# Kernel tuning notes

Measured on AMD Instinct MI355X. Metric: run time of the kernel, lower is better.

## Reference

```python
import jax, jax.numpy as jnp
import numpy as np

B, T, C = 4, 2048, 1024
H = 16
HD = C // H  # 64


def setup_inputs() -> dict:
    key = jax.random.key(0)
    k1, k2, k3 = jax.random.split(key, 3)
    x = jax.random.normal(k1, (B, T, C), dtype=jnp.float32)
    # learned params (torch Linear y = x @ W.T stored here as [in, out])
    Wqkv = jax.random.normal(k2, (C, 3 * C), dtype=jnp.float32) * (C ** -0.5)
    Wout = jax.random.normal(k3, (C, C), dtype=jnp.float32) * (C ** -0.5)
    bout = jnp.zeros((C,), dtype=jnp.float32)
    causal_mask = jnp.tril(jnp.ones((1, 1, T, T), dtype=bool))
    return {"x": x, "causal_mask": causal_mask, "Wqkv": Wqkv, "Wout": Wout, "bout": bout}


def reference(x, causal_mask, Wqkv, Wout, bout):
    b, t, c = x.shape
    scale = HD ** -0.5
    qkv = x @ Wqkv  # [B,T,3C]
    q, k, v = jnp.split(qkv, 3, axis=-1)
    # [B,T,C] -> [B,H,T,hd]
    q = q.reshape(b, t, H, HD).transpose(0, 2, 1, 3)
    k = k.reshape(b, t, H, HD).transpose(0, 2, 1, 3)
    v = v.reshape(b, t, H, HD).transpose(0, 2, 1, 3)
    att = jnp.einsum("bhqd,bhkd->bhqk", q, k) * scale  # [B,H,T,T]
    att = jnp.where(causal_mask, att, -jnp.inf)
    att = jax.nn.softmax(att, axis=-1)
    # dropout in eval mode == identity
    out = jnp.einsum("bhqk,bhkd->bhqd", att, v)  # [B,H,T,hd]
    out = out.transpose(0, 2, 1, 3).reshape(b, t, c)
    return out @ Wout + bout


if __name__ == "__main__":
    inp = setup_inputs()
    y = jax.jit(reference)(**inp)
    print(y.shape, y.dtype)
```

## Files before the change

kernel.cpp:

```cpp
#include <hip/hip_runtime.h>
#include <hip/hip_bf16.h>
#include <stdint.h>


typedef __bf16 bf16;
typedef __bf16 bf16x4 __attribute__((ext_vector_type(4)));
typedef __bf16 bf16x8 __attribute__((ext_vector_type(8)));
typedef float floatx4 __attribute__((ext_vector_type(4)));

#define MFMA16(a, b, c) __builtin_amdgcn_mfma_f32_16x16x32_bf16(a, b, c, 0, 0, 0)

#if defined(__has_builtin)
#if __has_builtin(__builtin_amdgcn_global_load_lds)
#define HAS_GLL 1
#endif
#endif

#ifdef HAS_GLL
__device__ __forceinline__ void gll16(const bf16* g, bf16* l) {
  __builtin_amdgcn_global_load_lds(
      (const __attribute__((address_space(1))) unsigned int*)g,
      (__attribute__((address_space(3))) unsigned int*)l, 16, 0, 0);
}
#endif

__global__ __launch_bounds__(256)
void convert_x(const float* __restrict__ in, bf16* __restrict__ out) {
  const size_t i = (size_t)blockIdx.x * 256 + threadIdx.x;
  const float4* p = (const float4*)in + i * 2;
  float4 a = p[0], b = p[1];
  bf16x8 v;
  v[0] = (bf16)a.x; v[1] = (bf16)a.y; v[2] = (bf16)a.z; v[3] = (bf16)a.w;
  v[4] = (bf16)b.x; v[5] = (bf16)b.y; v[6] = (bf16)b.z; v[7] = (bf16)b.w;
  *((bf16x8*)out + i) = v;
}

__global__ __launch_bounds__(256)
void transpose_w(const float* __restrict__ W, bf16* __restrict__ Wt, int K, int N) {
  __shared__ bf16 tile[32][33];
  const int k0 = blockIdx.y * 32, n0 = blockIdx.x * 32;
  const int t = threadIdx.x;
  {
    const int r = t >> 3, c4 = (t & 7) * 4;
    float4 v = *(const float4*)(W + (size_t)(k0 + r) * N + n0 + c4);
    tile[r][c4 + 0] = (bf16)v.x;
    tile[r][c4 + 1] = (bf16)v.y;
    tile[r][c4 + 2] = (bf16)v.z;
    tile[r][c4 + 3] = (bf16)v.w;
  }
  __syncthreads();
  {
    const int nr = t >> 3, kc = (t & 7) * 4;
    bf16x4 o;
#pragma unroll
    for (int j = 0; j < 4; ++j) o[j] = tile[kc + j][nr];
    *(bf16x4*)(Wt + (size_t)(n0 + nr) * K + k0 + kc) = o;
  }
}

__global__ __launch_bounds__(256)
void vtrans(const bf16* __restrict__ qkv, bf16* __restrict__ vtp) {
  __shared__ bf16 tile[64][72];
  const int t = threadIdx.x;
  const int kb = blockIdx.x * 64;
  const int bh = blockIdx.y;
  const int b = bh >> 4, h = bh & 15;
  const bf16* Vp = qkv + (size_t)b * 2048 * 3072 + 2048 + h * 64;
#pragma unroll
  for (int i = 0; i < 2; ++i) {
    const int c = t + 256 * i, kk = c >> 3, dg = c & 7;
    *(bf16x8*)(&tile[kk][dg * 8]) =
        *(const bf16x8*)(Vp + (size_t)(kb + kk) * 3072 + dg * 8);
  }
  __syncthreads();
#pragma unroll
  for (int i = 0; i < 2; ++i) {
    const int c = t + 256 * i, d = c >> 3, g = c & 7;
    bf16x8 v;
#pragma unroll
    for (int j = 0; j < 8; ++j) v[j] = tile[g * 8 + j][d];
    *(bf16x8*)(vtp + ((size_t)bh * 64 + d) * 2048 + kb + g * 8) = v;
  }
}

template <bool OUT_BF16>
__global__ __launch_bounds__(256, 3)
void gemm_bt(const bf16* __restrict__ A, const bf16* __restrict__ Bt,
             const float* __restrict__ bias, void* __restrict__ Cv,
             int M, int N, int K) {
  __shared__ __align__(16) bf16 As[128 * 64];
  __shared__ __align__(16) bf16 Bs[128 * 64];

  const int t = threadIdx.x, lane = t & 63, w = t >> 6;
  const int m_ = lane & 15, quad = lane >> 4;
  const int wm = w >> 1, wn = w & 1;
  const int m0 = blockIdx.y * 128, n0 = blockIdx.x * 128;

  floatx4 acc[4][4];
#pragma unroll
  for (int i = 0; i < 4; ++i)
#pragma unroll
    for (int j = 0; j < 4; ++j) {
      floatx4 z = {0.f, 0.f, 0.f, 0.f};
      acc[i][j] = z;
    }

  for (int k0 = 0; k0 < K; k0 += 64) {
#pragma unroll
    for (int i = 0; i < 4; ++i) {
      const int R0 = i * 32 + w * 8;
      const int R = R0 + (lane >> 3);
      const int sg = (lane & 7) ^ (R & 7);
      const bf16* ga = A + (size_t)(m0 + R) * K + k0 + sg * 8;
      const bf16* gb = Bt + (size_t)(n0 + R) * K + k0 + sg * 8;
#ifdef HAS_GLL
      gll16(ga, As + (size_t)R0 * 64);
      gll16(gb, Bs + (size_t)R0 * 64);
#else
      *(bf16x8*)(As + (size_t)R * 64 + (lane & 7) * 8) = *(const bf16x8*)ga;
      *(bf16x8*)(Bs + (size_t)R * 64 + (lane & 7) * 8) = *(const bf16x8*)gb;
#endif
    }
    __syncthreads();

#pragma unroll
    for (int kc = 0; kc < 2; ++kc) {
      bf16x8 af[4], bfr[4];
#pragma unroll
      for (int mt = 0; mt < 4; ++mt) {
        const int r = wm * 64 + mt * 16 + m_;
        const int slot = ((kc << 2) | quad) ^ (r & 7);
        af[mt] = *(const bf16x8*)(As + (size_t)r * 64 + slot * 8);
      }
#pragma unroll
      for (int nt = 0; nt < 4; ++nt) {
        const int rn = wn * 64 + nt * 16 + m_;
        const int slot = ((kc << 2) | quad) ^ (rn & 7);
        bfr[nt] = *(const bf16x8*)(Bs + (size_t)rn * 64 + slot * 8);
      }
#pragma unroll
      for (int mt = 0; mt < 4; ++mt)
#pragma unroll
        for (int nt = 0; nt < 4; ++nt)
          acc[mt][nt] = MFMA16(af[mt], bfr[nt], acc[mt][nt]);
    }
    __syncthreads();
  }

#pragma unroll
  for (int mt = 0; mt < 4; ++mt)
#pragma unroll
    for (int nt = 0; nt < 4; ++nt) {
      const int col = n0 + wn * 64 + nt * 16 + m_;
      const float bv = bias ? bias[col] : 0.f;
#pragma unroll
      for (int r = 0; r < 4; ++r) {
        const int row = m0 + wm * 64 + mt * 16 + quad * 4 + r;
        const float val = acc[mt][nt][r] + bv;
        if (OUT_BF16)
          ((bf16*)Cv)[(size_t)row * N + col] = (bf16)val;
        else
          ((float*)Cv)[(size_t)row * N + col] = val;
      }
    }
}

__global__ __launch_bounds__(256, 2)
void attn_fwd(const bf16* __restrict__ qkv, const bf16* __restrict__ vtp,
              bf16* __restrict__ attnout) {
  constexpr int KS = 72;
  constexpr float L2E = 1.44269504f;
  __shared__ __align__(16) bf16 Ks[64 * KS];
  __shared__ __align__(16) bf16 VT[64 * KS];
  __shared__ __align__(16) bf16 Pl[128 * KS];

  const int t = threadIdx.x, lane = t & 63, w = t >> 6;
  const int m_ = lane & 15, quad = lane >> 4;
  const int bh = blockIdx.x;
  const int pb = blockIdx.y;
  const int b = bh >> 4, h = bh & 15;
  const int srcbase = (lane & 48) + ((lane & 48) >> 2);

  const bf16* base = qkv + (size_t)b * 2048 * 3072;
  const bf16* Qp = base + h * 64;
  const bf16* Kp = base + 1024 + h * 64;
  const bf16* Vt = vtp + (size_t)bh * 64 * 2048;

  const int sr0 = t >> 3, sg0 = t & 7;
  const int sr1 = (t + 256) >> 3, sg1 = t & 7;

#pragma unroll
  for (int pass = 0; pass < 2; ++pass) {
    const int qb = pass ? (15 - pb) : pb;
    const int q0w = qb * 128 + w * 32;

    bf16x8 qf[2][2];
#pragma unroll
    for (int mt = 0; mt < 2; ++mt)
#pragma unroll
      for (int kc = 0; kc < 2; ++kc)
        qf[mt][kc] = *(const bf16x8*)(Qp + (size_t)(q0w + mt * 16 + m_) * 3072 +
                                      kc * 32 + quad * 8);

    floatx4 o[2][4];
#pragma unroll
    for (int mt = 0; mt < 2; ++mt)
#pragma unroll
      for (int nt = 0; nt < 4; ++nt) {
        floatx4 z = {0.f, 0.f, 0.f, 0.f};
        o[mt][nt] = z;
      }
    float mrow[2] = {-1e30f, -1e30f}, lrow[2] = {0.f, 0.f};

    const int nch = 2 * qb + 2;

    bf16x8 kr0, kr1, vr0, vr1;
    kr0 = *(const bf16x8*)(Kp + (size_t)sr0 * 3072 + sg0 * 8);
    kr1 = *(const bf16x8*)(Kp + (size_t)sr1 * 3072 + sg1 * 8);
    vr0 = *(const bf16x8*)(Vt + (size_t)sr0 * 2048 + sg0 * 8);
    vr1 = *(const bf16x8*)(Vt + (size_t)sr1 * 2048 + sg1 * 8);

    for (int ch = 0; ch < nch; ++ch) {
      const int kb = ch * 64;
      __syncthreads();
      *(bf16x8*)(Ks + (size_t)sr0 * KS + sg0 * 8) = kr0;
      *(bf16x8*)(Ks + (size_t)sr1 * KS + sg1 * 8) = kr1;
      *(bf16x8*)(VT + (size_t)sr0 * KS + sg0 * 8) = vr0;
      *(bf16x8*)(VT + (size_t)sr1 * KS + sg1 * 8) = vr1;
      __syncthreads();
      if (ch + 1 < nch) {
        const int kn = kb + 64;
        kr0 = *(const bf16x8*)(Kp + (size_t)(kn + sr0) * 3072 + sg0 * 8);
        kr1 = *(const bf16x8*)(Kp + (size_t)(kn + sr1) * 3072 + sg1 * 8);
        vr0 = *(const bf16x8*)(Vt + (size_t)sr0 * 2048 + kn + sg0 * 8);
        vr1 = *(const bf16x8*)(Vt + (size_t)sr1 * 2048 + kn + sg1 * 8);
      }

      if (kb <= q0w + 31) {
        bf16x8 kf[4][2];
#pragma unroll
        for (int kt = 0; kt < 4; ++kt)
#pragma unroll
          for (int kc = 0; kc < 2; ++kc)
            kf[kt][kc] = *(const bf16x8*)(Ks + (size_t)(kt * 16 + m_) * KS +
                                          kc * 32 + quad * 8);
        const bool need_mask = (kb + 63 > q0w);
#pragma unroll
        for (int mt = 0; mt < 2; ++mt) {
          floatx4 s[4];
#pragma unroll
          for (int kt = 0; kt < 4; ++kt) {
            floatx4 z = {0.f, 0.f, 0.f, 0.f};
            z = MFMA16(kf[kt][0], qf[mt][0], z);
            z = MFMA16(kf[kt][1], qf[mt][1], z);
            s[kt] = z;
          }
          float a[4][4];
#pragma unroll
          for (int kt = 0; kt < 4; ++kt)
#pragma unroll
            for (int r = 0; r < 4; ++r) a[kt][r] = s[kt][r] * (0.125f * L2E);
          if (need_mask) {
            const int qglob = q0w + mt * 16 + m_;
#pragma unroll
            for (int kt = 0; kt < 4; ++kt)
#pragma unroll
              for (int r = 0; r < 4; ++r)
                if (kb + kt * 16 + quad * 4 + r > qglob) a[kt][r] = -1e30f;
          }
          float mx = -1e30f;
#pragma unroll
          for (int kt = 0; kt < 4; ++kt)
#pragma unroll
            for (int r = 0; r < 4; ++r) mx = fmaxf(mx, a[kt][r]);
          mx = fmaxf(mx, __shfl_xor(mx, 16));
          mx = fmaxf(mx, __shfl_xor(mx, 32));
          const float mnew = fmaxf(mrow[mt], mx);
          const float alpha = exp2f(mrow[mt] - mnew);
          mrow[mt] = mnew;
          float psum = 0.f;
#pragma unroll
          for (int kt = 0; kt < 4; ++kt) {
            bf16x4 pw;
#pragma unroll
            for (int r = 0; r < 4; ++r) {
              const float p = exp2f(a[kt][r] - mnew);
              psum += p;
              pw[r] = (bf16)p;
            }
            *(bf16x4*)(Pl + (size_t)((w * 2 + mt) * 16 + m_) * KS + kt * 16 +
                       quad * 4) = pw;
          }
          psum += __shfl_xor(psum, 16);
          psum += __shfl_xor(psum, 32);
          lrow[mt] = lrow[mt] * alpha + psum;
#pragma unroll
          for (int r = 0; r < 4; ++r) {
            const float ar = __shfl(alpha, srcbase + r);
#pragma unroll
            for (int nt = 0; nt < 4; ++nt) o[mt][nt][r] *= ar;
          }
        }
        bf16x8 vf[4][2];
#pragma unroll
        for (int nt = 0; nt < 4; ++nt)
#pragma unroll
          for (int kc = 0; kc < 2; ++kc)
            vf[nt][kc] = *(const bf16x8*)(VT + (size_t)(nt * 16 + m_) * KS +
                                          kc * 32 + quad * 8);
#pragma unroll
        for (int mt = 0; mt < 2; ++mt) {
          const bf16* prow = Pl + (size_t)((w * 2 + mt) * 16 + m_) * KS;
          const bf16x8 pf0 = *(const bf16x8*)(prow + quad * 8);
          const bf16x8 pf1 = *(const bf16x8*)(prow + 32 + quad * 8);
#pragma unroll
          for (int nt = 0; nt < 4; ++nt) {
            o[mt][nt] = MFMA16(pf0, vf[nt][0], o[mt][nt]);
            o[mt][nt] = MFMA16(pf1, vf[nt][1], o[mt][nt]);
          }
        }
      }
    }
    __syncthreads();

#pragma unroll
    for (int mt = 0; mt < 2; ++mt) {
      const float linv = 1.0f / lrow[mt];
#pragma unroll
      for (int r = 0; r < 4; ++r) {
        const float inv = __shfl(linv, srcbase + r);
        const int row = q0w + mt * 16 + quad * 4 + r;
        const size_t orow = ((size_t)b * 2048 + row) * 1024 + h * 64;
#pragma unroll
        for (int nt = 0; nt < 4; ++nt)
          attnout[orow + nt * 16 + m_] = (bf16)(o[mt][nt][r] * inv);
      }
    }
  }
}

extern "C" void kernel_launch(void* const* d_in, const int* in_sizes, int n_in,
                              void* d_out, int out_size, void* d_ws, size_t ws_size,
                              hipStream_t stream) {
  (void)in_sizes; (void)n_in; (void)out_size; (void)ws_size;
  const float* x    = (const float*)d_in[0];
  const float* Wqkv = (const float*)d_in[2];
  const float* Wout = (const float*)d_in[3];
  const float* bout = (const float*)d_in[4];
  float* out = (float*)d_out;

  bf16* qkv     = (bf16*)d_ws;
  bf16* attnout = (bf16*)((char*)d_ws + (size_t)8192 * 3072 * 2);
  bf16* Wout_t  = (bf16*)d_ws;
  bf16* xbf    = (bf16*)d_out;
  bf16* Wqkv_t = (bf16*)d_out + (size_t)8192 * 1024;
  bf16* vtp    = (bf16*)d_out + (size_t)8192 * 1024;

  convert_x<<<4096, 256, 0, stream>>>(x, xbf);
  transpose_w<<<dim3(96, 32), 256, 0, stream>>>(Wqkv, Wqkv_t, 1024, 3072);

  gemm_bt<true><<<dim3(24, 64), 256, 0, stream>>>(xbf, Wqkv_t, nullptr, qkv,
                                                  8192, 3072, 1024);
  vtrans<<<dim3(32, 64), 256, 0, stream>>>(qkv, vtp);
  attn_fwd<<<dim3(64, 8), 256, 0, stream>>>(qkv, vtp, attnout);

  transpose_w<<<dim3(32, 32), 256, 0, stream>>>(Wout, Wout_t, 1024, 1024);
  gemm_bt<false><<<dim3(8, 64), 256, 0, stream>>>(attnout, Wout_t, bout, out,
                                                  8192, 1024, 1024);
}
```

Measured before the change: 281.9 us.

## Fuse V transpose into QKV GEMM epilogue, prescale Q, skip unneeded rescales

The QKV GEMM epilogue now writes Q (prescaled by softmax scale times log2e) and K into a compact buffer and writes V directly in transposed per-head layout, removing the separate vtrans kernel. The attention kernel drops its per-score scaling multiply and only rescales the output accumulator when some row max grew in the wave. The transposed V stores are strided and less coalesced, and prescaling Q before bf16 rounding slightly changes numerics.

```diff
diff --git a/kernel.cpp b/kernel.cpp
--- a/kernel.cpp
+++ b/kernel.cpp
@@ -58,36 +58,11 @@
   }
 }
 
-__global__ __launch_bounds__(256)
-void vtrans(const bf16* __restrict__ qkv, bf16* __restrict__ vtp) {
-  __shared__ bf16 tile[64][72];
-  const int t = threadIdx.x;
-  const int kb = blockIdx.x * 64;
-  const int bh = blockIdx.y;
-  const int b = bh >> 4, h = bh & 15;
-  const bf16* Vp = qkv + (size_t)b * 2048 * 3072 + 2048 + h * 64;
-#pragma unroll
-  for (int i = 0; i < 2; ++i) {
-    const int c = t + 256 * i, kk = c >> 3, dg = c & 7;
-    *(bf16x8*)(&tile[kk][dg * 8]) =
-        *(const bf16x8*)(Vp + (size_t)(kb + kk) * 3072 + dg * 8);
-  }
-  __syncthreads();
-#pragma unroll
-  for (int i = 0; i < 2; ++i) {
-    const int c = t + 256 * i, d = c >> 3, g = c & 7;
-    bf16x8 v;
-#pragma unroll
-    for (int j = 0; j < 8; ++j) v[j] = tile[g * 8 + j][d];
-    *(bf16x8*)(vtp + ((size_t)bh * 64 + d) * 2048 + kb + g * 8) = v;
-  }
-}
-
-template <bool OUT_BF16>
+template <int MODE>
 __global__ __launch_bounds__(256, 3)
 void gemm_bt(const bf16* __restrict__ A, const bf16* __restrict__ Bt,
              const float* __restrict__ bias, void* __restrict__ Cv,
-             int M, int N, int K) {
+             bf16* __restrict__ Vout, int M, int N, int K) {
   __shared__ __align__(16) bf16 As[128 * 64];
   __shared__ __align__(16) bf16 Bs[128 * 64];
 
@@ -147,29 +122,56 @@
     __syncthreads();
   }
 
-#pragma unroll
-  for (int mt = 0; mt < 4; ++mt)
-#pragma unroll
-    for (int nt = 0; nt < 4; ++nt) {
-      const int col = n0 + wn * 64 + nt * 16 + m_;
-      const float bv = bias ? bias[col] : 0.f;
-#pragma unroll
-      for (int r = 0; r < 4; ++r) {
-        const int row = m0 + wm * 64 + mt * 16 + quad * 4 + r;
-        const float val = acc[mt][nt][r] + bv;
-        if (OUT_BF16)
-          ((bf16*)Cv)[(size_t)row * N + col] = (bf16)val;
-        else
-          ((float*)Cv)[(size_t)row * N + col] = val;
-      }
-    }
+  if (MODE == 0) {
+#pragma unroll
+    for (int mt = 0; mt < 4; ++mt)
+#pragma unroll
+      for (int nt = 0; nt < 4; ++nt) {
+        const int col = n0 + wn * 64 + nt * 16 + m_;
+        const float bv = bias[col];
+#pragma unroll
+        for (int r = 0; r < 4; ++r) {
+          const int row = m0 + wm * 64 + mt * 16 + quad * 4 + r;
+          ((float*)Cv)[(size_t)row * N + col] = acc[mt][nt][r] + bv;
+        }
+      }
+  } else {
+    if (n0 < 2048) {
+      const float sc = (n0 < 1024) ? 0.18033688f : 1.0f;
+#pragma unroll
+      for (int mt = 0; mt < 4; ++mt)
+#pragma unroll
+        for (int nt = 0; nt < 4; ++nt) {
+          const int col = n0 + wn * 64 + nt * 16 + m_;
+#pragma unroll
+          for (int r = 0; r < 4; ++r) {
+            const int row = m0 + wm * 64 + mt * 16 + quad * 4 + r;
+            ((bf16*)Cv)[(size_t)row * 2048 + col] = (bf16)(acc[mt][nt][r] * sc);
+          }
+        }
+    } else {
+#pragma unroll
+      for (int mt = 0; mt < 4; ++mt) {
+        const int rowb = m0 + wm * 64 + mt * 16 + quad * 4;
+        const int bb = rowb >> 11, tok = rowb & 2047;
+#pragma unroll
+        for (int nt = 0; nt < 4; ++nt) {
+          const int c = n0 - 2048 + wn * 64 + nt * 16 + m_;
+          const int h = c >> 6, d = c & 63;
+          bf16x4 pw;
+#pragma unroll
+          for (int r = 0; r < 4; ++r) pw[r] = (bf16)acc[mt][nt][r];
+          *(bf16x4*)(Vout + ((size_t)(bb * 16 + h) * 64 + d) * 2048 + tok) = pw;
+        }
+      }
+    }
+  }
 }
 
 __global__ __launch_bounds__(256, 2)
-void attn_fwd(const bf16* __restrict__ qkv, const bf16* __restrict__ vtp,
+void attn_fwd(const bf16* __restrict__ qk, const bf16* __restrict__ vtp,
               bf16* __restrict__ attnout) {
   constexpr int KS = 72;
-  constexpr float L2E = 1.44269504f;
   __shared__ __align__(16) bf16 Ks[64 * KS];
   __shared__ __align__(16) bf16 VT[64 * KS];
   __shared__ __align__(16) bf16 Pl[128 * KS];
@@ -181,9 +183,8 @@
   const int b = bh >> 4, h = bh & 15;
   const int srcbase = (lane & 48) + ((lane & 48) >> 2);
 
-  const bf16* base = qkv + (size_t)b * 2048 * 3072;
-  const bf16* Qp = base + h * 64;
-  const bf16* Kp = base + 1024 + h * 64;
+  const bf16* Qp = qk + (size_t)b * 2048 * 2048 + h * 64;
+  const bf16* Kp = qk + (size_t)b * 2048 * 2048 + 1024 + h * 64;
   const bf16* Vt = vtp + (size_t)bh * 64 * 2048;
 
   const int sr0 = t >> 3, sg0 = t & 7;
@@ -199,7 +200,7 @@
     for (int mt = 0; mt < 2; ++mt)
 #pragma unroll
       for (int kc = 0; kc < 2; ++kc)
-        qf[mt][kc] = *(const bf16x8*)(Qp + (size_t)(q0w + mt * 16 + m_) * 3072 +
+        qf[mt][kc] = *(const bf16x8*)(Qp + (size_t)(q0w + mt * 16 + m_) * 2048 +
                                       kc * 32 + quad * 8);
 
     floatx4 o[2][4];
@@ -215,8 +216,8 @@
     const int nch = 2 * qb + 2;
 
     bf16x8 kr0, kr1, vr0, vr1;
-    kr0 = *(const bf16x8*)(Kp + (size_t)sr0 * 3072 + sg0 * 8);
-    kr1 = *(const bf16x8*)(Kp + (size_t)sr1 * 3072 + sg1 * 8);
+    kr0 = *(const bf16x8*)(Kp + (size_t)sr0 * 2048 + sg0 * 8);
+    kr1 = *(const bf16x8*)(Kp + (size_t)sr1 * 2048 + sg1 * 8);
     vr0 = *(const bf16x8*)(Vt + (size_t)sr0 * 2048 + sg0 * 8);
     vr1 = *(const bf16x8*)(Vt + (size_t)sr1 * 2048 + sg1 * 8);
 
@@ -230,8 +231,8 @@
       __syncthreads();
       if (ch + 1 < nch) {
         const int kn = kb + 64;
-        kr0 = *(const bf16x8*)(Kp + (size_t)(kn + sr0) * 3072 + sg0 * 8);
-        kr1 = *(const bf16x8*)(Kp + (size_t)(kn + sr1) * 3072 + sg1 * 8);
+        kr0 = *(const bf16x8*)(Kp + (size_t)(kn + sr0) * 2048 + sg0 * 8);
+        kr1 = *(const bf16x8*)(Kp + (size_t)(kn + sr1) * 2048 + sg1 * 8);
         vr0 = *(const bf16x8*)(Vt + (size_t)sr0 * 2048 + kn + sg0 * 8);
         vr1 = *(const bf16x8*)(Vt + (size_t)sr1 * 2048 + kn + sg1 * 8);
       }
@@ -259,7 +260,7 @@
 #pragma unroll
           for (int kt = 0; kt < 4; ++kt)
 #pragma unroll
-            for (int r = 0; r < 4; ++r) a[kt][r] = s[kt][r] * (0.125f * L2E);
+            for (int r = 0; r < 4; ++r) a[kt][r] = s[kt][r];
           if (need_mask) {
             const int qglob = q0w + mt * 16 + m_;
 #pragma unroll
@@ -268,16 +269,16 @@
               for (int r = 0; r < 4; ++r)
                 if (kb + kt * 16 + quad * 4 + r > qglob) a[kt][r] = -1e30f;
           }
-          float mx = -1e30f;
+          float m4[4];
 #pragma unroll
           for (int kt = 0; kt < 4; ++kt)
-#pragma unroll
-            for (int r = 0; r < 4; ++r) mx = fmaxf(mx, a[kt][r]);
+            m4[kt] = fmaxf(fmaxf(a[kt][0], a[kt][1]), fmaxf(a[kt][2], a[kt][3]));
+          float mx = fmaxf(fmaxf(m4[0], m4[1]), fmaxf(m4[2], m4[3]));
           mx = fmaxf(mx, __shfl_xor(mx, 16));
           mx = fmaxf(mx, __shfl_xor(mx, 32));
-          const float mnew = fmaxf(mrow[mt], mx);
-          const float alpha = exp2f(mrow[mt] - mnew);
-          mrow[mt] = mnew;
+          const float mold = mrow[mt];
+          const float mnew = fmaxf(mold, mx);
+          const bool grew = mnew > mold;
           float psum = 0.f;
 #pragma unroll
           for (int kt = 0; kt < 4; ++kt) {
@@ -293,12 +294,18 @@
           }
           psum += __shfl_xor(psum, 16);
           psum += __shfl_xor(psum, 32);
-          lrow[mt] = lrow[mt] * alpha + psum;
-#pragma unroll
-          for (int r = 0; r < 4; ++r) {
-            const float ar = __shfl(alpha, srcbase + r);
-#pragma unroll
-            for (int nt = 0; nt < 4; ++nt) o[mt][nt][r] *= ar;
+          if (__any(grew)) {
+            const float alpha = exp2f(mold - mnew);
+            lrow[mt] = lrow[mt] * alpha + psum;
+            mrow[mt] = mnew;
+#pragma unroll
+            for (int r = 0; r < 4; ++r) {
+              const float ar = __shfl(alpha, srcbase + r);
+#pragma unroll
+              for (int nt = 0; nt < 4; ++nt) o[mt][nt][r] *= ar;
+            }
+          } else {
+            lrow[mt] += psum;
           }
         }
         bf16x8 vf[4][2];
@@ -349,22 +356,21 @@
   const float* bout = (const float*)d_in[4];
   float* out = (float*)d_out;
 
-  bf16* qkv     = (bf16*)d_ws;
-  bf16* attnout = (bf16*)((char*)d_ws + (size_t)8192 * 3072 * 2);
+  bf16* qk      = (bf16*)d_ws;
+  bf16* vtp     = (bf16*)((char*)d_ws + (size_t)32 * 1024 * 1024);
+  bf16* attnout = (bf16*)((char*)d_ws + (size_t)48 * 1024 * 1024);
   bf16* Wout_t  = (bf16*)d_ws;
   bf16* xbf    = (bf16*)d_out;
   bf16* Wqkv_t = (bf16*)d_out + (size_t)8192 * 1024;
-  bf16* vtp    = (bf16*)d_out + (size_t)8192 * 1024;
 
   convert_x<<<4096, 256, 0, stream>>>(x, xbf);
   transpose_w<<<dim3(96, 32), 256, 0, stream>>>(Wqkv, Wqkv_t, 1024, 3072);
 
-  gemm_bt<true><<<dim3(24, 64), 256, 0, stream>>>(xbf, Wqkv_t, nullptr, qkv,
-                                                  8192, 3072, 1024);
-  vtrans<<<dim3(32, 64), 256, 0, stream>>>(qkv, vtp);
-  attn_fwd<<<dim3(64, 8), 256, 0, stream>>>(qkv, vtp, attnout);
+  gemm_bt<1><<<dim3(24, 64), 256, 0, stream>>>(xbf, Wqkv_t, nullptr, qk, vtp,
+                                               8192, 3072, 1024);
+  attn_fwd<<<dim3(64, 8), 256, 0, stream>>>(qk, vtp, attnout);
 
   transpose_w<<<dim3(32, 32), 256, 0, stream>>>(Wout, Wout_t, 1024, 1024);
-  gemm_bt<false><<<dim3(8, 64), 256, 0, stream>>>(attnout, Wout_t, bout, out,
-                                                  8192, 1024, 1024);
-}
+  gemm_bt<0><<<dim3(8, 64), 256, 0, stream>>>(attnout, Wout_t, bout, out,
+                                              nullptr, 8192, 1024, 1024);
+}
```

Result: faster. 275.4 us (-2.3%).
